# Performance work log

Measured on AMD Instinct MI355X. Metric: run time of the kernel, lower is better.

Reference implementation:

```python
import jax, jax.numpy as jnp
import numpy as np

B, S, D, H = 2, 2048, 2048, 16
HD = D // H
THETA = 10000.0


def _rope(t, pos):
    # t: [B, H, S, hd], pos: [S] int -> rotary position embedding (half-split form)
    half = t.shape[-1] // 2
    inv_freq = 1.0 / (THETA ** (jnp.arange(half, dtype=jnp.float32) / half))
    ang = pos[:, None].astype(jnp.float32) * inv_freq[None, :]  # [S, half]
    cos, sin = jnp.cos(ang), jnp.sin(ang)
    t1, t2 = t[..., :half], t[..., half:]
    return jnp.concatenate([t1 * cos - t2 * sin, t1 * sin + t2 * cos], axis=-1)


def setup_inputs() -> dict:
    key = jax.random.key(0)
    ks = jax.random.split(key, 5)
    scale = 1.0 / np.sqrt(D)
    return {
        "x": jax.random.normal(ks[0], (B, S, D), dtype=jnp.float32),
        "Wq": jax.random.normal(ks[1], (D, D), dtype=jnp.float32) * scale,
        "Wk": jax.random.normal(ks[2], (D, D), dtype=jnp.float32) * scale,
        "Wv": jax.random.normal(ks[3], (D, D), dtype=jnp.float32) * scale,
        "Wo": jax.random.normal(ks[4], (D, D), dtype=jnp.float32) * scale,
        "token_positions": jnp.arange(S, dtype=jnp.int32),
    }


def reference(x, Wq, Wk, Wv, Wo, token_positions):
    b, s, d = x.shape
    # fused QKV projection (nn.Linear: y = x @ W.T)
    q = (x @ Wq.T).reshape(b, s, H, HD).transpose(0, 2, 1, 3)  # [B,H,S,hd]
    k = (x @ Wk.T).reshape(b, s, H, HD).transpose(0, 2, 1, 3)
    v = (x @ Wv.T).reshape(b, s, H, HD).transpose(0, 2, 1, 3)
    q = _rope(q, token_positions)
    k = _rope(k, token_positions)
    scale = 1.0 / np.sqrt(HD)
    scores = jnp.einsum("bhqd,bhkd->bhqk", q, k) * scale  # [B,H,S,S]
    causal = jnp.triu(jnp.ones((s, s), dtype=bool), k=1)
    scores = jnp.where(causal, jnp.float32(-jnp.inf), scores)
    attn = jax.nn.softmax(scores, axis=-1)
    o = jnp.einsum("bhqk,bhkd->bhqd", attn, v)  # [B,H,S,hd]
    o = o.transpose(0, 2, 1, 3).reshape(b, s, d)
    return o @ Wo.T
```

## Files before the change

kernel.cpp:

```cpp
#include <hip/hip_runtime.h>
#include <math.h>

#define B_  2
#define S_  2048
#define D_  2048
#define H_  16
#define HD_ 128

using u16 = unsigned short;
using u32 = unsigned int;
typedef __attribute__((ext_vector_type(4))) float f32x4;
typedef __attribute__((ext_vector_type(8))) short bf16x8;
using u16x4_t = __attribute__((ext_vector_type(4))) unsigned short;
using u16x8_t = __attribute__((ext_vector_type(8))) unsigned short;
typedef __attribute__((ext_vector_type(2))) u32 u32x2;
typedef __attribute__((ext_vector_type(4))) u32 u32x4;

__device__ __forceinline__ u16 f2bf(float f) {
  u32 u = __builtin_bit_cast(u32, f);
  u32 r = u + 0x7fffu + ((u >> 16) & 1u);
  return (u16)(r >> 16);
}
__device__ __forceinline__ float bf2f(u16 x) {
  u32 u = ((u32)x) << 16;
  return __builtin_bit_cast(float, u);
}
__device__ __forceinline__ void async_copy16(const u16* g, u16* l) {
  __builtin_amdgcn_global_load_lds((const __attribute__((address_space(1))) u32*)g,
                                   (__attribute__((address_space(3))) u32*)l, 16, 0, 0);
}

__global__ void cvt_f32_bf16(const float* __restrict__ src, u16* __restrict__ dst, int n) {
  int i = (blockIdx.x * blockDim.x + threadIdx.x) * 4;
  if (i >= n) return;
  float4 v = *(const float4*)(src + i);
  u16x4_t o;
  o[0] = f2bf(v.x); o[1] = f2bf(v.y); o[2] = f2bf(v.z); o[3] = f2bf(v.w);
  *(u16x4_t*)(dst + i) = o;
}

__global__ void rope_table(const int* __restrict__ pos, float2* __restrict__ tab) {
  int t = blockIdx.x * blockDim.x + threadIdx.x;
  if (t >= S_ * 64) return;
  int s = t >> 6, i = t & 63;
  float freq = expf(-(float)i * (9.210340371976184f / 64.0f));
  float ang = (float)pos[s] * freq;
  tab[t] = make_float2(cosf(ang), sinf(ang));
}

__global__ void rope_apply(u16* __restrict__ Q, u16* __restrict__ K,
                           const float2* __restrict__ tab) {
  int t = blockIdx.x * blockDim.x + threadIdx.x;
  int g = t & 15;
  int bsh = t >> 4;
  int h = bsh & (H_ - 1);
  int bs = bsh >> 4;
  int s = bs & (S_ - 1);
  size_t base = (size_t)bs * D_ + (size_t)h * HD_;
  int d2 = g * 4;
  const float2* tb = &tab[s * 64 + d2];
  float2 cs[4];
  #pragma unroll
  for (int j = 0; j < 4; ++j) cs[j] = tb[j];
  #pragma unroll
  for (int which = 0; which < 2; ++which) {
    u16* P = which ? K : Q;
    u16x4_t a = *(u16x4_t*)(P + base + d2);
    u16x4_t c = *(u16x4_t*)(P + base + 64 + d2);
    u16x4_t ra, rc;
    #pragma unroll
    for (int j = 0; j < 4; ++j) {
      float t1 = bf2f(a[j]), t2 = bf2f(c[j]);
      ra[j] = f2bf(t1 * cs[j].x - t2 * cs[j].y);
      rc[j] = f2bf(t1 * cs[j].y + t2 * cs[j].x);
    }
    *(u16x4_t*)(P + base + d2) = ra;
    *(u16x4_t*)(P + base + 64 + d2) = rc;
  }
}

template <bool F32OUT>
__global__ void gemm_bt(const u16* __restrict__ A, const u16* __restrict__ Bt,
                        void* __restrict__ Cout, int M, int N, int K) {
  __shared__ u16 lA[3][128 * 32];
  __shared__ u16 lB[3][128 * 32];
  const int tid = threadIdx.x;
  const int lane = tid & 63;
  const int w = tid >> 6;
  const int wr = w >> 1, wc = w & 1;
  const int bm = blockIdx.x * 128;
  const int bn = blockIdx.y * 128;
  const int fr = lane & 15, fq = lane >> 4;
  const int KT = K >> 5;
  f32x4 acc[4][4] = {};

  auto stage = [&](int buf, int kt) {
    const int k0 = kt << 5;
    #pragma unroll
    for (int c = w; c < 8; c += 4) {
      const int r = c * 16 + (lane >> 2);
      const int col = ((lane & 3) ^ ((r >> 1) & 3)) * 8;
      async_copy16(A + (size_t)(bm + r) * K + k0 + col, &lA[buf][c * 512]);
      async_copy16(Bt + (size_t)(bn + r) * K + k0 + col, &lB[buf][c * 512]);
    }
  };

  stage(0, 0);
  stage(1, 1);
  asm volatile("s_waitcnt vmcnt(4)" ::: "memory");
  __builtin_amdgcn_s_barrier();
  asm volatile("" ::: "memory");

  int p = 0, sb = 2;
  #pragma unroll 1
  for (int kt = 0; kt < KT; ++kt) {
    if (kt + 2 < KT) stage(sb, kt + 2);
    bf16x8 af[4], bfr[4];
    #pragma unroll
    for (int i = 0; i < 4; ++i) {
      const int ra = wr * 64 + i * 16 + fr;
      const int rb = wc * 64 + i * 16 + fr;
      af[i]  = *(const bf16x8*)&lA[p][ra * 32 + ((fq ^ ((ra >> 1) & 3)) * 8)];
      bfr[i] = *(const bf16x8*)&lB[p][rb * 32 + ((fq ^ ((rb >> 1) & 3)) * 8)];
    }
    #pragma unroll
    for (int i = 0; i < 4; ++i)
      #pragma unroll
      for (int j = 0; j < 4; ++j)
        acc[i][j] = __builtin_amdgcn_mfma_f32_16x16x32_bf16(af[i], bfr[j], acc[i][j], 0, 0, 0);
    if (kt + 1 < KT) {
      if (kt + 2 < KT) asm volatile("s_waitcnt vmcnt(4)" ::: "memory");
      else             asm volatile("s_waitcnt vmcnt(0)" ::: "memory");
      __builtin_amdgcn_s_barrier();
      asm volatile("" ::: "memory");
    }
    p  = (p == 2) ? 0 : p + 1;
    sb = (sb == 2) ? 0 : sb + 1;
  }
  #pragma unroll
  for (int i = 0; i < 4; ++i)
    #pragma unroll
    for (int j = 0; j < 4; ++j) {
      const int row = bm + wr * 64 + i * 16 + fq * 4;
      const int col = bn + wc * 64 + j * 16 + fr;
      #pragma unroll
      for (int r = 0; r < 4; ++r) {
        const float v = acc[i][j][r];
        if (F32OUT) ((float*)Cout)[(size_t)(row + r) * N + col] = v;
        else        ((u16*)Cout)[(size_t)(row + r) * N + col] = f2bf(v);
      }
    }
}

__global__ void gemm_qkv3(const u16* __restrict__ A, const u16* __restrict__ Bt,
                          u16* __restrict__ Qo, u16* __restrict__ Ko, u16* __restrict__ Vo) {
  __shared__ u16 lA[3][128 * 32];
  __shared__ u16 lB[3][128 * 32];
  const int tid = threadIdx.x;
  const int lane = tid & 63;
  const int w = tid >> 6;
  const int wr = w >> 1, wc = w & 1;
  const int bm = blockIdx.x * 128;
  const int bn = blockIdx.y * 128;
  const int fr = lane & 15, fq = lane >> 4;
  const int K = D_;
  const int KT = K >> 5;
  f32x4 acc[4][4] = {};

  auto stage = [&](int buf, int kt) {
    const int k0 = kt << 5;
    #pragma unroll
    for (int c = w; c < 8; c += 4) {
      const int r = c * 16 + (lane >> 2);
      const int col = ((lane & 3) ^ ((r >> 1) & 3)) * 8;
      async_copy16(A + (size_t)(bm + r) * K + k0 + col, &lA[buf][c * 512]);
      async_copy16(Bt + (size_t)(bn + r) * K + k0 + col, &lB[buf][c * 512]);
    }
  };

  stage(0, 0);
  stage(1, 1);
  asm volatile("s_waitcnt vmcnt(4)" ::: "memory");
  __builtin_amdgcn_s_barrier();
  asm volatile("" ::: "memory");

  int p = 0, sb = 2;
  #pragma unroll 1
  for (int kt = 0; kt < KT; ++kt) {
    if (kt + 2 < KT) stage(sb, kt + 2);
    bf16x8 af[4], bfr[4];
    #pragma unroll
    for (int i = 0; i < 4; ++i) {
      const int ra = wr * 64 + i * 16 + fr;
      const int rb = wc * 64 + i * 16 + fr;
      af[i]  = *(const bf16x8*)&lA[p][ra * 32 + ((fq ^ ((ra >> 1) & 3)) * 8)];
      bfr[i] = *(const bf16x8*)&lB[p][rb * 32 + ((fq ^ ((rb >> 1) & 3)) * 8)];
    }
    #pragma unroll
    for (int i = 0; i < 4; ++i)
      #pragma unroll
      for (int j = 0; j < 4; ++j)
        acc[i][j] = __builtin_amdgcn_mfma_f32_16x16x32_bf16(af[i], bfr[j], acc[i][j], 0, 0, 0);
    if (kt + 1 < KT) {
      if (kt + 2 < KT) asm volatile("s_waitcnt vmcnt(4)" ::: "memory");
      else             asm volatile("s_waitcnt vmcnt(0)" ::: "memory");
      __builtin_amdgcn_s_barrier();
      asm volatile("" ::: "memory");
    }
    p  = (p == 2) ? 0 : p + 1;
    sb = (sb == 2) ? 0 : sb + 1;
  }
  u16* out = (bn < 2048) ? Qo : (bn < 4096) ? Ko : Vo;
  const int bnl = bn & 2047;
  #pragma unroll
  for (int i = 0; i < 4; ++i)
    #pragma unroll
    for (int j = 0; j < 4; ++j) {
      const int row = bm + wr * 64 + i * 16 + fq * 4;
      const int col = bnl + wc * 64 + j * 16 + fr;
      #pragma unroll
      for (int r = 0; r < 4; ++r)
        out[(size_t)(row + r) * D_ + col] = f2bf(acc[i][j][r]);
    }
}

#define QB 64
#define KB 32
#define PLD 36

__global__ __launch_bounds__(256, 2)
void attn_fwd(const u16* __restrict__ Qg, const u16* __restrict__ Kg,
              const u16* __restrict__ Vg, u16* __restrict__ po0,
              u16* __restrict__ po1, float2* __restrict__ ml) {
  __shared__ u16 lK[2][KB * HD_];
  __shared__ u16 lV[2][HD_ * 40];
  __shared__ u16 lP[4][16 * PLD];
  const int tid = threadIdx.x;
  const int lane = tid & 63;
  const int w = tid >> 6;
  const int fr = lane & 15, fq = lane >> 4;
  const int bh = blockIdx.y;
  const int split = blockIdx.z;
  const size_t base = (size_t)(bh >> 4) * S_ * D_ + (size_t)(bh & 15) * HD_;
  const int xA = blockIdx.x;
  const int qA = xA * QB, qB = (31 - xA) * QB;
  const int ntA = (qA + QB) / KB;
  const int ntB = (qB + QB) / KB;
  const int c = (ntA <= 16) ? (33 - ntA) : 16;
  const int t0 = split ? c : 0;
  const int t1 = split ? ntB : c;
  const float kscale = 0.08838834764831843f * 1.4426950408889634f;

  bf16x8 qfA[4], qfB[4];
  {
    const u16* qpa = Qg + base + (size_t)(qA + w * 16 + fr) * D_ + fq * 8;
    const u16* qpb = Qg + base + (size_t)(qB + w * 16 + fr) * D_ + fq * 8;
    #pragma unroll
    for (int kk = 0; kk < 4; ++kk) {
      qfA[kk] = *(const bf16x8*)(qpa + kk * 32);
      qfB[kk] = *(const bf16x8*)(qpb + kk * 32);
    }
  }
  f32x4 oA[8] = {}, oB[8] = {};
  float mAs = -INFINITY, lAs = 0.f, mBs = -INFINITY, lBs = 0.f;

  auto stageK = [&](int buf, int kv0) {
    #pragma unroll
    for (int cc = w; cc < 8; cc += 4) {
      const int row = cc * 4 + (lane >> 4);
      const int slot = (lane & 15) ^ (row & 7);
      async_copy16(Kg + base + (size_t)(kv0 + row) * D_ + slot * 8, &lK[buf][cc * 512]);
    }
  };
  const int srow = tid >> 3, sc0 = (tid & 7) * 16;
  const u32 swz = (u32)((sc0 >> 4) & 7) << 4;
  const u32 rb = (u32)srow * 2;
  u16x8_t rv0, rv1;
  auto loadV = [&](int kv0) {
    const u16* gv = Vg + base + (size_t)(kv0 + srow) * D_ + sc0;
    rv0 = *(const u16x8_t*)gv; rv1 = *(const u16x8_t*)(gv + 8);
  };
  auto writeV = [&](int buf) {
    char* lv = (char*)&lV[buf][0];
    #pragma unroll
    for (int j = 0; j < 8; ++j) {
      *(u16*)(lv + ((((u32)(sc0 + j) * 80) + rb) ^ swz))     = rv0[j];
      *(u16*)(lv + ((((u32)(sc0 + 8 + j) * 80) + rb) ^ swz)) = rv1[j];
    }
  };

  auto softmax_sw = [&](const f32x4& s0, const f32x4& s1, float& mrow, float& lrow,
                        f32x4* o, int q0t, int kv0) {
    const int qg = q0t + w * 16 + fr;
    const bool notfull = (kv0 + KB - 1 > q0t);
    float v[8];
    #pragma unroll
    for (int r = 0; r < 4; ++r) {
      v[r]     = s0[r] * kscale;
      v[4 + r] = s1[r] * kscale;
      if (notfull) {
        if (kv0 + fq * 4 + r > qg)      v[r]     = -INFINITY;
        if (kv0 + 16 + fq * 4 + r > qg) v[4 + r] = -INFINITY;
      }
    }
    float mx = fmaxf(fmaxf(fmaxf(v[0], v[1]), fmaxf(v[2], v[3])),
                     fmaxf(fmaxf(v[4], v[5]), fmaxf(v[6], v[7])));
    mx = fmaxf(mx, __shfl_xor(mx, 16));
    mx = fmaxf(mx, __shfl_xor(mx, 32));
    const float mn = fmaxf(mrow, mx);
    const float al = exp2f(mrow - mn);
    mrow = mn;
    float p[8];
    #pragma unroll
    for (int j = 0; j < 8; ++j) p[j] = exp2f(v[j] - mn);
    float rs = ((p[0] + p[1]) + (p[2] + p[3])) + ((p[4] + p[5]) + (p[6] + p[7]));
    rs += __shfl_xor(rs, 16);
    rs += __shfl_xor(rs, 32);
    lrow = lrow * al + rs;
    #pragma unroll
    for (int r = 0; r < 4; ++r) {
      lP[w][fr * PLD + fq * 4 + r]      = f2bf(p[r]);
      lP[w][fr * PLD + 16 + fq * 4 + r] = f2bf(p[4 + r]);
    }
    #pragma unroll
    for (int r = 0; r < 4; ++r) {
      const float ab = __shfl(al, fq * 4 + r);
      #pragma unroll
      for (int nb = 0; nb < 8; ++nb) o[nb][r] *= ab;
    }
  };

  auto pv = [&](f32x4* o, const bf16x8* vf) {
    u32x2 pa0 = *(const u32x2*)&lP[w][fr * PLD + fq * 8];
    u32x2 pa1 = *(const u32x2*)&lP[w][fr * PLD + fq * 8 + 4];
    u32x4 pc; pc[0] = pa0[0]; pc[1] = pa0[1]; pc[2] = pa1[0]; pc[3] = pa1[1];
    const bf16x8 pa = __builtin_bit_cast(bf16x8, pc);
    #pragma unroll
    for (int nb = 0; nb < 8; ++nb)
      o[nb] = __builtin_amdgcn_mfma_f32_16x16x32_bf16(pa, vf[nb], o[nb], 0, 0, 0);
  };

  stageK(0, t0 * KB);
  loadV(t0 * KB);
  writeV(0);

  for (int t = t0; t < t1; ++t) {
    const int kv0 = t * KB;
    const int cur = (t - t0) & 1, nxt = cur ^ 1;
    __syncthreads();
    if (t + 1 < t1) {
      stageK(nxt, kv0 + KB);
      loadV(kv0 + KB);
    }

    const bool doA = (t < ntA);
    f32x4 sA0 = {}, sA1 = {}, sB0 = {}, sB1 = {};
    #pragma unroll
    for (int kk = 0; kk < 4; ++kk) {
      const int sl = ((kk * 4 + fq) ^ (fr & 7)) * 16;
      bf16x8 k0f = *(const bf16x8*)((const char*)&lK[cur][0] + fr * 256 + sl);
      bf16x8 k1f = *(const bf16x8*)((const char*)&lK[cur][0] + (16 + fr) * 256 + sl);
      if (doA) {
        sA0 = __builtin_amdgcn_mfma_f32_16x16x32_bf16(k0f, qfA[kk], sA0, 0, 0, 0);
        sA1 = __builtin_amdgcn_mfma_f32_16x16x32_bf16(k1f, qfA[kk], sA1, 0, 0, 0);
      }
      sB0 = __builtin_amdgcn_mfma_f32_16x16x32_bf16(k0f, qfB[kk], sB0, 0, 0, 0);
      sB1 = __builtin_amdgcn_mfma_f32_16x16x32_bf16(k1f, qfB[kk], sB1, 0, 0, 0);
    }

    bf16x8 vf[8];
    #pragma unroll
    for (int nb = 0; nb < 8; ++nb) {
      const u32 off = (((u32)(nb * 16 + fr) * 80) + (u32)fq * 16) ^ ((u32)nb << 4);
      vf[nb] = *(const bf16x8*)((const char*)&lV[cur][0] + off);
    }

    if (doA) { softmax_sw(sA0, sA1, mAs, lAs, oA, qA, kv0); pv(oA, vf); }
    softmax_sw(sB0, sB1, mBs, lBs, oB, qB, kv0);
    pv(oB, vf);

    if (t + 1 < t1) writeV(nxt);
  }

  u16* po = split ? po1 : po0;
  float2* mlp = ml + (size_t)split * (B_ * H_ * S_) + (size_t)bh * S_;
  if (lane < 16) {
    mlp[qA + w * 16 + fr] = make_float2(mAs, lAs);
    mlp[qB + w * 16 + fr] = make_float2(mBs, lBs);
  }
  #pragma unroll
  for (int r = 0; r < 4; ++r) {
    const int rowA = qA + w * 16 + fq * 4 + r;
    const int rowB = qB + w * 16 + fq * 4 + r;
    u16* orA = po + base + (size_t)rowA * D_;
    u16* orB = po + base + (size_t)rowB * D_;
    #pragma unroll
    for (int nb = 0; nb < 8; ++nb) {
      orA[nb * 16 + fr] = f2bf(oA[nb][r]);
      orB[nb * 16 + fr] = f2bf(oB[nb][r]);
    }
  }
}

__global__ void attn_combine(const u16* __restrict__ po0, const u16* __restrict__ po1,
                             const float2* __restrict__ ml, u16* __restrict__ Og) {
  const int idx = blockIdx.x * blockDim.x + threadIdx.x;
  const int d8 = (idx & 15) * 8;
  const int row = idx >> 4;
  const int bh = row >> 11, s = row & (S_ - 1);
  const float2 v0 = ml[row];
  const float2 v1 = ml[B_ * H_ * S_ + row];
  const float m = fmaxf(v0.x, v1.x);
  const float e0 = exp2f(v0.x - m), e1 = exp2f(v1.x - m);
  const float inv = 1.0f / (v0.y * e0 + v1.y * e1);
  const size_t off = (size_t)(bh >> 4) * S_ * D_ + (size_t)s * D_ + (bh & 15) * HD_ + d8;
  u16x8_t a = *(const u16x8_t*)(po0 + off);
  u16x8_t b = *(const u16x8_t*)(po1 + off);
  u16x8_t o;
  #pragma unroll
  for (int j = 0; j < 8; ++j)
    o[j] = f2bf((bf2f(a[j]) * e0 + bf2f(b[j]) * e1) * inv);
  *(u16x8_t*)(Og + off) = o;
}

extern "C" void kernel_launch(void* const* d_in, const int* in_sizes, int n_in,
                              void* d_out, int out_size, void* d_ws, size_t ws_size,
                              hipStream_t stream) {
  const float* x  = (const float*)d_in[0];
  const float* Wq = (const float*)d_in[1];
  const float* Wk = (const float*)d_in[2];
  const float* Wv = (const float*)d_in[3];
  const float* Wo = (const float*)d_in[4];
  const int* pos  = (const int*)d_in[5];

  char* p = (char*)d_ws;
  u16* xb  = (u16*)p; p += (size_t)B_ * S_ * D_ * 2;
  u16* Wqb = (u16*)p; p += (size_t)D_ * D_ * 2;
  u16* Wkb = (u16*)p; p += (size_t)D_ * D_ * 2;
  u16* Wvb = (u16*)p; p += (size_t)D_ * D_ * 2;
  u16* Wob = (u16*)p; p += (size_t)D_ * D_ * 2;
  u16* Qb  = (u16*)p; p += (size_t)B_ * S_ * D_ * 2;
  u16* Kb  = (u16*)p; p += (size_t)B_ * S_ * D_ * 2;
  u16* Vb  = (u16*)p; p += (size_t)B_ * S_ * D_ * 2;
  float2* tab = (float2*)p; p += (size_t)S_ * 64 * sizeof(float2);
  float2* ml  = (float2*)p; p += (size_t)2 * B_ * H_ * S_ * sizeof(float2);
  u16* po0 = xb;
  u16* po1 = Wqb;
  u16* Ob  = Qb;

  const int nx = B_ * S_ * D_;
  const int nw = D_ * D_;
  cvt_f32_bf16<<<nx / 1024, 256, 0, stream>>>(x,  xb,  nx);
  cvt_f32_bf16<<<nw / 1024, 256, 0, stream>>>(Wq, Wqb, nw);
  cvt_f32_bf16<<<nw / 1024, 256, 0, stream>>>(Wk, Wkb, nw);
  cvt_f32_bf16<<<nw / 1024, 256, 0, stream>>>(Wv, Wvb, nw);
  cvt_f32_bf16<<<nw / 1024, 256, 0, stream>>>(Wo, Wob, nw);
  rope_table<<<(S_ * 64) / 256, 256, 0, stream>>>(pos, tab);

  gemm_qkv3<<<dim3(B_ * S_ / 128, 48), 256, 0, stream>>>(xb, Wqb, Qb, Kb, Vb);

  rope_apply<<<(B_ * S_ * H_ * 16) / 256, 256, 0, stream>>>(Qb, Kb, tab);

  attn_fwd<<<dim3(16, B_ * H_, 2), 256, 0, stream>>>(Qb, Kb, Vb, po0, po1, ml);
  attn_combine<<<(B_ * H_ * S_ * 16) / 256, 256, 0, stream>>>(po0, po1, ml, Ob);

  gemm_bt<true><<<dim3(B_ * S_ / 128, D_ / 128), 256, 0, stream>>>(Ob, Wob, (float*)d_out, B_ * S_, D_, D_);
}
```

Baseline: 328.0 us.

## Fuse RoPE into QKV epilogue and attention Q load, merge conversions, remap workgroups

Removes the standalone rope_apply kernel. RoPE for K is now applied in the QKV GEMM epilogue, with partner halves exchanged through LDS, and RoPE for Q is applied in registers when the attention kernel loads Q. The five f32->bf16 conversion launches are merged into one kernel. Workgroup IDs in both GEMMs and in attention are remapped (XCD-style interleave by 8) to improve L2 locality across chiplets. In exchange, the K-tile epilogue gains extra LDS traffic and barriers, and Q is rounded to bf16 twice.

```diff
diff --git a/kernel.cpp b/kernel.cpp
--- a/kernel.cpp
+++ b/kernel.cpp
@@ -30,10 +30,21 @@
                                    (__attribute__((address_space(3))) u32*)l, 16, 0, 0);
 }
 
-__global__ void cvt_f32_bf16(const float* __restrict__ src, u16* __restrict__ dst, int n) {
-  int i = (blockIdx.x * blockDim.x + threadIdx.x) * 4;
-  if (i >= n) return;
-  float4 v = *(const float4*)(src + i);
+__global__ void cvt_all(const float* __restrict__ x, const float* __restrict__ Wq,
+                        const float* __restrict__ Wk, const float* __restrict__ Wv,
+                        const float* __restrict__ Wo, u16* __restrict__ dst) {
+  const int i = (blockIdx.x * blockDim.x + threadIdx.x) * 4;
+  if (i >= 25165824) return;
+  const float* src;
+  int off;
+  if (i < (1 << 23)) { src = x; off = i; }
+  else {
+    const int wi = i - (1 << 23);
+    const int which = wi >> 22;
+    off = wi & ((1 << 22) - 1);
+    src = (which == 0) ? Wq : (which == 1) ? Wk : (which == 2) ? Wv : Wo;
+  }
+  float4 v = *(const float4*)(src + off);
   u16x4_t o;
   o[0] = f2bf(v.x); o[1] = f2bf(v.y); o[2] = f2bf(v.z); o[3] = f2bf(v.w);
   *(u16x4_t*)(dst + i) = o;
@@ -46,37 +57,6 @@
   float freq = expf(-(float)i * (9.210340371976184f / 64.0f));
   float ang = (float)pos[s] * freq;
   tab[t] = make_float2(cosf(ang), sinf(ang));
-}
-
-__global__ void rope_apply(u16* __restrict__ Q, u16* __restrict__ K,
-                           const float2* __restrict__ tab) {
-  int t = blockIdx.x * blockDim.x + threadIdx.x;
-  int g = t & 15;
-  int bsh = t >> 4;
-  int h = bsh & (H_ - 1);
-  int bs = bsh >> 4;
-  int s = bs & (S_ - 1);
-  size_t base = (size_t)bs * D_ + (size_t)h * HD_;
-  int d2 = g * 4;
-  const float2* tb = &tab[s * 64 + d2];
-  float2 cs[4];
-  #pragma unroll
-  for (int j = 0; j < 4; ++j) cs[j] = tb[j];
-  #pragma unroll
-  for (int which = 0; which < 2; ++which) {
-    u16* P = which ? K : Q;
-    u16x4_t a = *(u16x4_t*)(P + base + d2);
-    u16x4_t c = *(u16x4_t*)(P + base + 64 + d2);
-    u16x4_t ra, rc;
-    #pragma unroll
-    for (int j = 0; j < 4; ++j) {
-      float t1 = bf2f(a[j]), t2 = bf2f(c[j]);
-      ra[j] = f2bf(t1 * cs[j].x - t2 * cs[j].y);
-      rc[j] = f2bf(t1 * cs[j].y + t2 * cs[j].x);
-    }
-    *(u16x4_t*)(P + base + d2) = ra;
-    *(u16x4_t*)(P + base + 64 + d2) = rc;
-  }
 }
 
 template <bool F32OUT>
@@ -88,8 +68,11 @@
   const int lane = tid & 63;
   const int w = tid >> 6;
   const int wr = w >> 1, wc = w & 1;
-  const int bm = blockIdx.x * 128;
-  const int bn = blockIdx.y * 128;
+  const int nwg = gridDim.x * gridDim.y;
+  int lid = blockIdx.y * gridDim.x + blockIdx.x;
+  lid = (lid & 7) * (nwg >> 3) + (lid >> 3);
+  const int bm = (lid % gridDim.x) * 128;
+  const int bn = (lid / gridDim.x) * 128;
   const int fr = lane & 15, fq = lane >> 4;
   const int KT = K >> 5;
   f32x4 acc[4][4] = {};
@@ -153,6 +136,7 @@
 }
 
 __global__ void gemm_qkv3(const u16* __restrict__ A, const u16* __restrict__ Bt,
+                          const float2* __restrict__ tab,
                           u16* __restrict__ Qo, u16* __restrict__ Ko, u16* __restrict__ Vo) {
   __shared__ u16 lA[3][128 * 32];
   __shared__ u16 lB[3][128 * 32];
@@ -160,8 +144,10 @@
   const int lane = tid & 63;
   const int w = tid >> 6;
   const int wr = w >> 1, wc = w & 1;
-  const int bm = blockIdx.x * 128;
-  const int bn = blockIdx.y * 128;
+  int lid = blockIdx.y * gridDim.x + blockIdx.x;
+  lid = (lid & 7) * 192 + (lid >> 3);
+  const int bm = (lid & 31) * 128;
+  const int bn = (lid >> 5) * 128;
   const int fr = lane & 15, fq = lane >> 4;
   const int K = D_;
   const int KT = K >> 5;
@@ -210,18 +196,49 @@
     p  = (p == 2) ? 0 : p + 1;
     sb = (sb == 2) ? 0 : sb + 1;
   }
-  u16* out = (bn < 2048) ? Qo : (bn < 4096) ? Ko : Vo;
+
   const int bnl = bn & 2047;
-  #pragma unroll
-  for (int i = 0; i < 4; ++i)
-    #pragma unroll
-    for (int j = 0; j < 4; ++j) {
-      const int row = bm + wr * 64 + i * 16 + fq * 4;
-      const int col = bnl + wc * 64 + j * 16 + fr;
-      #pragma unroll
-      for (int r = 0; r < 4; ++r)
-        out[(size_t)(row + r) * D_ + col] = f2bf(acc[i][j][r]);
-    }
+  if (bn >= 2048 && bn < 4096) {
+    float* xch = (float*)&lA[0][0];
+    float* myslot = xch + (size_t)(w * 64 + lane) * 17;
+    float* pslot  = xch + (size_t)((w ^ 1) * 64 + lane) * 17;
+    __syncthreads();
+    #pragma unroll 1
+    for (int i = 0; i < 4; ++i) {
+      #pragma unroll
+      for (int j = 0; j < 4; ++j)
+        #pragma unroll
+        for (int r = 0; r < 4; ++r) myslot[j * 4 + r] = acc[i][j][r];
+      __syncthreads();
+      #pragma unroll
+      for (int j = 0; j < 4; ++j) {
+        const int fi = j * 16 + fr;
+        #pragma unroll
+        for (int r = 0; r < 4; ++r) {
+          const int row = bm + wr * 64 + i * 16 + fq * 4 + r;
+          const float2 cs = tab[(row & (S_ - 1)) * 64 + fi];
+          const float own = acc[i][j][r];
+          const float par = pslot[j * 4 + r];
+          const float v = wc ? (par * cs.y + own * cs.x)
+                             : (own * cs.x - par * cs.y);
+          Ko[(size_t)row * D_ + (bnl + wc * 64 + j * 16 + fr)] = f2bf(v);
+        }
+      }
+      if (i < 3) __syncthreads();
+    }
+  } else {
+    u16* out = (bn < 2048) ? Qo : Vo;
+    #pragma unroll
+    for (int i = 0; i < 4; ++i)
+      #pragma unroll
+      for (int j = 0; j < 4; ++j) {
+        const int row = bm + wr * 64 + i * 16 + fq * 4;
+        const int col = bnl + wc * 64 + j * 16 + fr;
+        #pragma unroll
+        for (int r = 0; r < 4; ++r)
+          out[(size_t)(row + r) * D_ + col] = f2bf(acc[i][j][r]);
+      }
+  }
 }
 
 #define QB 64
@@ -230,8 +247,8 @@
 
 __global__ __launch_bounds__(256, 2)
 void attn_fwd(const u16* __restrict__ Qg, const u16* __restrict__ Kg,
-              const u16* __restrict__ Vg, u16* __restrict__ po0,
-              u16* __restrict__ po1, float2* __restrict__ ml) {
+              const u16* __restrict__ Vg, const float2* __restrict__ tab,
+              u16* __restrict__ po0, u16* __restrict__ po1, float2* __restrict__ ml) {
   __shared__ u16 lK[2][KB * HD_];
   __shared__ u16 lV[2][HD_ * 40];
   __shared__ u16 lP[4][16 * PLD];
@@ -239,10 +256,12 @@
   const int lane = tid & 63;
   const int w = tid >> 6;
   const int fr = lane & 15, fq = lane >> 4;
-  const int bh = blockIdx.y;
-  const int split = blockIdx.z;
+  int lid = blockIdx.z * 512 + blockIdx.y * 16 + blockIdx.x;
+  lid = (lid & 7) * 128 + (lid >> 3);
+  const int xA = lid & 15;
+  const int bh = (lid >> 4) & 31;
+  const int split = lid >> 9;
   const size_t base = (size_t)(bh >> 4) * S_ * D_ + (size_t)(bh & 15) * HD_;
-  const int xA = blockIdx.x;
   const int qA = xA * QB, qB = (31 - xA) * QB;
   const int ntA = (qA + QB) / KB;
   const int ntB = (qB + QB) / KB;
@@ -260,6 +279,21 @@
       qfA[kk] = *(const bf16x8*)(qpa + kk * 32);
       qfB[kk] = *(const bf16x8*)(qpb + kk * 32);
     }
+    const float2* tA = &tab[(qA + w * 16 + fr) * 64 + fq * 8];
+    const float2* tB = &tab[(qB + w * 16 + fr) * 64 + fq * 8];
+    #pragma unroll
+    for (int kk = 0; kk < 2; ++kk)
+      #pragma unroll
+      for (int j = 0; j < 8; ++j) {
+        const float2 ca = tA[kk * 32 + j];
+        float t1 = bf2f((u16)qfA[kk][j]), t2 = bf2f((u16)qfA[kk + 2][j]);
+        qfA[kk][j]     = (short)f2bf(t1 * ca.x - t2 * ca.y);
+        qfA[kk + 2][j] = (short)f2bf(t1 * ca.y + t2 * ca.x);
+        const float2 cb = tB[kk * 32 + j];
+        t1 = bf2f((u16)qfB[kk][j]); t2 = bf2f((u16)qfB[kk + 2][j]);
+        qfB[kk][j]     = (short)f2bf(t1 * cb.x - t2 * cb.y);
+        qfB[kk + 2][j] = (short)f2bf(t1 * cb.y + t2 * cb.x);
+      }
   }
   f32x4 oA[8] = {}, oB[8] = {};
   float mAs = -INFINITY, lAs = 0.f, mBs = -INFINITY, lBs = 0.f;
@@ -448,20 +482,12 @@
   u16* po1 = Wqb;
   u16* Ob  = Qb;
 
-  const int nx = B_ * S_ * D_;
-  const int nw = D_ * D_;
-  cvt_f32_bf16<<<nx / 1024, 256, 0, stream>>>(x,  xb,  nx);
-  cvt_f32_bf16<<<nw / 1024, 256, 0, stream>>>(Wq, Wqb, nw);
-  cvt_f32_bf16<<<nw / 1024, 256, 0, stream>>>(Wk, Wkb, nw);
-  cvt_f32_bf16<<<nw / 1024, 256, 0, stream>>>(Wv, Wvb, nw);
-  cvt_f32_bf16<<<nw / 1024, 256, 0, stream>>>(Wo, Wob, nw);
+  cvt_all<<<24576, 256, 0, stream>>>(x, Wq, Wk, Wv, Wo, xb);
   rope_table<<<(S_ * 64) / 256, 256, 0, stream>>>(pos, tab);
 
-  gemm_qkv3<<<dim3(B_ * S_ / 128, 48), 256, 0, stream>>>(xb, Wqb, Qb, Kb, Vb);
-
-  rope_apply<<<(B_ * S_ * H_ * 16) / 256, 256, 0, stream>>>(Qb, Kb, tab);
-
-  attn_fwd<<<dim3(16, B_ * H_, 2), 256, 0, stream>>>(Qb, Kb, Vb, po0, po1, ml);
+  gemm_qkv3<<<dim3(B_ * S_ / 128, 48), 256, 0, stream>>>(xb, Wqb, tab, Qb, Kb, Vb);
+
+  attn_fwd<<<dim3(16, B_ * H_, 2), 256, 0, stream>>>(Qb, Kb, Vb, tab, po0, po1, ml);
   attn_combine<<<(B_ * H_ * S_ * 16) / 256, 256, 0, stream>>>(po0, po1, ml, Ob);
 
   gemm_bt<true><<<dim3(B_ * S_ / 128, D_ / 128), 256, 0, stream>>>(Ob, Wob, (float*)d_out, B_ * S_, D_, D_);
```

After: 389.2 us. +18.6%, slower.
